# Kernel tuning notes

Hardware: AMD Instinct MI355X
Metric: run time of the kernel (lower is better)

## Reference

```python
import jax, jax.numpy as jnp
import numpy as np

B, N, D, H = 8, 2048, 768, 12
HD = D // H
SCALE = HD ** -0.5


def setup_inputs() -> dict:
    key = jax.random.key(0)
    ks = jax.random.split(key, 5)
    std = D ** -0.5
    return {
        "x": jax.random.normal(ks[0], (B, N, D), jnp.float32),
        "W_qkv": jax.random.normal(ks[1], (D, 3 * D), jnp.float32) * std,
        "b_qkv": jax.random.normal(ks[2], (3 * D,), jnp.float32) * 0.02,
        "W_out": jax.random.normal(ks[3], (D, D), jnp.float32) * std,
        "b_out": jax.random.normal(ks[4], (D,), jnp.float32) * 0.02,
    }


def reference(x, W_qkv, b_qkv, W_out, b_out):
    qkv = x @ W_qkv + b_qkv
    qkv = qkv.reshape(B, N, 3, H, HD).transpose(2, 0, 3, 1, 4)
    q, k, v = qkv[0], qkv[1], qkv[2]
    # scaled dot-product attention (dropout is identity in eval)
    attn = jnp.einsum("bhqd,bhkd->bhqk", q, k) * SCALE
    attn = jax.nn.softmax(attn, axis=-1)
    out = jnp.einsum("bhqk,bhkd->bhqd", attn, v)
    out = out.transpose(0, 2, 1, 3).reshape(B, N, D)
    return out @ W_out + b_out
```

## Files before the change

### kernel.cpp

```cpp
#include <hip/hip_runtime.h>
#include <hip/hip_bf16.h>
#include <stdint.h>

#define BB 8
#define NN 2048
#define DD 768
#define HH 12
#define HD 64
#define ND3 2304
#define TOK (BB*NN)
#define QSC 0.18033688011112042f

typedef __bf16 bf16x8 __attribute__((ext_vector_type(8)));
typedef float  f32x4  __attribute__((ext_vector_type(4)));
typedef float  f32x16 __attribute__((ext_vector_type(16)));
typedef unsigned uint2v __attribute__((ext_vector_type(2)));

__device__ __forceinline__ unsigned short f2bf(float f) {
    union { float f; unsigned u; } v; v.f = f;
    unsigned r = v.u + 0x7FFF + ((v.u >> 16) & 1);
    return (unsigned short)(r >> 16);
}
__device__ __forceinline__ unsigned packbf(float lo, float hi) {
    return __builtin_amdgcn_perm(__float_as_uint(hi) + 0x8000u,
                                 __float_as_uint(lo) + 0x8000u, 0x07060302u);
}
__device__ __forceinline__ unsigned cvtpk(float lo, float hi) {
    unsigned r;
    asm("v_cvt_pk_bf16_f32 %0, %1, %2" : "=v"(r) : "v"(lo), "v"(hi));
    return r;
}

__device__ __forceinline__ void gload_lds16(const unsigned short* g, unsigned short* l) {
    __builtin_amdgcn_global_load_lds((const __attribute__((address_space(1))) void*)g,
                                     (__attribute__((address_space(3))) void*)l, 16, 0, 0);
}

__global__ __launch_bounds__(256) void f32_to_bf16_vec(const float* __restrict__ in,
                                                       unsigned short* __restrict__ out, int n4) {
    int i = blockIdx.x * 256 + threadIdx.x;
    if (i < n4) {
        float4 v = reinterpret_cast<const float4*>(in)[i];
        ushort4 o;
        o.x = f2bf(v.x); o.y = f2bf(v.y); o.z = f2bf(v.z); o.w = f2bf(v.w);
        reinterpret_cast<ushort4*>(out)[i] = o;
    }
}

__global__ __launch_bounds__(256) void transpose_bf16_tiled(const float* __restrict__ in,
                                                            unsigned short* __restrict__ out,
                                                            int R, int C) {
    __shared__ float t[32][33];
    const int tid = threadIdx.x;
    const int tc = tid & 31;
    const int tr = tid >> 5;
    const int r0 = blockIdx.y * 32;
    const int c0 = blockIdx.x * 32;
    #pragma unroll
    for (int j = 0; j < 4; ++j)
        t[tr + j * 8][tc] = in[(size_t)(r0 + tr + j * 8) * C + c0 + tc];
    __syncthreads();
    #pragma unroll
    for (int j = 0; j < 4; ++j)
        out[(size_t)(c0 + tr + j * 8) * R + r0 + tc] = f2bf(t[tc][tr + j * 8]);
}

__global__ __launch_bounds__(256) void qkv_gemm(const unsigned short* __restrict__ xb,
                                                const unsigned short* __restrict__ wt,
                                                const float* __restrict__ bias,
                                                unsigned short* __restrict__ qb,
                                                unsigned short* __restrict__ kb,
                                                unsigned short* __restrict__ vt) {
    __shared__ __align__(16) unsigned short As[2][128 * 32];
    __shared__ __align__(16) unsigned short Bs[2][128 * 32];
    const int tid  = threadIdx.x;
    const int wave = tid >> 6;
    const int lane = tid & 63;
    const int qd   = lane >> 4;
    const int c    = lane & 15;

    const int nbx  = gridDim.x;
    const int nwg  = nbx * gridDim.y;
    const int orig = blockIdx.y * nbx + blockIdx.x;
    const int swz  = (orig & 7) * (nwg >> 3) + (orig >> 3);
    const int m0 = (swz / nbx) * 128;
    const int n0 = (swz % nbx) * 128;

    const int wm = (wave >> 1) * 64;
    const int wn = (wave & 1) * 64;

    const unsigned short* Ag = xb + (size_t)(m0 + wave * 32 + (lane >> 2)) * DD + (lane & 3) * 8;
    const unsigned short* Bg = wt + (size_t)(n0 + wave * 32 + (lane >> 2)) * DD + (lane & 3) * 8;
    const int rb = wave * 32;

    #pragma unroll
    for (int j = 0; j < 2; ++j) {
        gload_lds16(Ag + (size_t)(j * 16) * DD, &As[0][(rb + j * 16) * 32]);
        gload_lds16(Bg + (size_t)(j * 16) * DD, &Bs[0][(rb + j * 16) * 32]);
    }
    __syncthreads();

    f32x4 acc[4][4] = {};
    #pragma unroll 1
    for (int t = 0; t < DD / 32; ++t) {
        const int cur = t & 1;
        if (t + 1 < DD / 32) {
            const int k1 = (t + 1) * 32;
            #pragma unroll
            for (int j = 0; j < 2; ++j) {
                gload_lds16(Ag + (size_t)(j * 16) * DD + k1, &As[cur ^ 1][(rb + j * 16) * 32]);
                gload_lds16(Bg + (size_t)(j * 16) * DD + k1, &Bs[cur ^ 1][(rb + j * 16) * 32]);
            }
        }
        bf16x8 a[4], b[4];
        #pragma unroll
        for (int i = 0; i < 4; ++i)
            a[i] = *reinterpret_cast<const bf16x8*>(&As[cur][(wm + i * 16 + c) * 32 + qd * 8]);
        #pragma unroll
        for (int j = 0; j < 4; ++j)
            b[j] = *reinterpret_cast<const bf16x8*>(&Bs[cur][(wn + j * 16 + c) * 32 + qd * 8]);
        __builtin_amdgcn_s_setprio(1);
        #pragma unroll
        for (int i = 0; i < 4; ++i)
            #pragma unroll
            for (int j = 0; j < 4; ++j)
                acc[i][j] = __builtin_amdgcn_mfma_f32_16x16x32_bf16(a[i], b[j], acc[i][j], 0, 0, 0);
        __builtin_amdgcn_s_setprio(0);
        __syncthreads();
    }

    const int tt  = n0 / DD;
    const int cw  = n0 - tt * DD + wn;
    const int hh  = cw >> 6;
    const int rowb = m0 + wm;
    const int bi  = rowb >> 11;
    const int nb  = rowb & (NN - 1);
    const float scale = (tt == 0) ? QSC : 1.0f;

    unsigned short* W = (wave < 2) ? (&As[0][0] + wave * 4096)
                                   : (&Bs[0][0] + (wave - 2) * 4096);

    #pragma unroll
    for (int i = 0; i < 4; ++i)
        #pragma unroll
        for (int j = 0; j < 4; ++j)
            #pragma unroll
            for (int r = 0; r < 4; ++r) {
                int lr = i * 16 + qd * 4 + r;
                int lc = j * 16 + c;
                float v = (acc[i][j][r] + bias[n0 + wn + lc]) * scale;
                int rr  = (tt == 2) ? lc : lr;
                int ccl = (tt == 2) ? lr : lc;
                W[rr * 64 + ((((ccl >> 3) ^ (rr & 7)) << 3) | (ccl & 7))] = f2bf(v);
            }

    const int lr8 = lane >> 3;
    const int lch = lane & 7;
    unsigned short* dst0;
    size_t rstride;
    if (tt == 2) {
        dst0 = vt + ((size_t)(bi * HH + hh) * HD) * NN + nb + lch * 8;
        rstride = NN;
    } else {
        unsigned short* qk = (tt == 0) ? qb : kb;
        dst0 = qk + ((size_t)(bi * HH + hh) * NN + nb) * HD + lch * 8;
        rstride = HD;
    }
    #pragma unroll
    for (int s = 0; s < 8; ++s) {
        int rr  = s * 8 + lr8;
        int pch = lch ^ (rr & 7);
        uint4 val = *reinterpret_cast<const uint4*>(W + rr * 64 + pch * 8);
        *reinterpret_cast<uint4*>(dst0 + (size_t)rr * rstride) = val;
    }
}

__global__ __launch_bounds__(256, 4) void attn_kernel(const unsigned short* __restrict__ qb,
                                                      const unsigned short* __restrict__ kb,
                                                      const unsigned short* __restrict__ vt,
                                                      unsigned short* __restrict__ ao) {
    __shared__ __align__(16) unsigned short Ks[2][64 * HD];
    __shared__ __align__(16) unsigned short Vs[2][64 * HD];

    const int blk  = blockIdx.x;
    const int xcd  = blk & 7;
    const int g    = blk >> 3;
    const int bh   = xcd * 12 + (g >> 4);
    const int qt   = g & 15;
    const int tid  = threadIdx.x;
    const int wave = tid >> 6;
    const int lane = tid & 63;
    const int col  = lane & 31;
    const int hf   = lane >> 5;
    const int q0   = qt * 128 + wave * 32;

    const unsigned short* Qp = qb + (size_t)bh * NN * HD;
    const unsigned short* Kp = kb + (size_t)bh * NN * HD;
    const unsigned short* Vp = vt + (size_t)bh * HD * NN;

    const int srow = lane >> 3;
    const int sch  = (lane & 7) ^ srow;

    const int cswz = col & 7;
    const int o0 = col * 128 + ((0 + hf) ^ cswz) * 16;
    const int o1 = col * 128 + ((2 + hf) ^ cswz) * 16;
    const int o2 = col * 128 + ((4 + hf) ^ cswz) * 16;
    const int o3 = col * 128 + ((6 + hf) ^ cswz) * 16;

    bf16x8 aq[4];
    #pragma unroll
    for (int ks = 0; ks < 4; ++ks)
        aq[ks] = *reinterpret_cast<const bf16x8*>(Qp + (size_t)(q0 + col) * HD + ks * 16 + hf * 8);

    f32x16 ot[2] = {};
    f32x16 lacc  = {};
    const f32x16 zf = {};

    union { unsigned short u[8]; bf16x8 v; } onesb;
    #pragma unroll
    for (int i = 0; i < 8; ++i) onesb.u[i] = 0x3F80;

    #pragma unroll
    for (int j = 0; j < 2; ++j) {
        const int rb = wave * 16 + j * 8;
        gload_lds16(Kp + (size_t)(rb + srow) * HD + sch * 8, &Ks[0][rb * HD]);
        gload_lds16(Vp + (size_t)(rb + srow) * NN + sch * 8, &Vs[0][rb * HD]);
    }
    __syncthreads();

    #pragma unroll 1
    for (int kt = 0; kt < NN; kt += 64) {
        const int cur = (kt >> 6) & 1;

        if (kt + 64 < NN) {
            const int nb = cur ^ 1;
            #pragma unroll
            for (int j = 0; j < 2; ++j) {
                const int rb = wave * 16 + j * 8;
                gload_lds16(Kp + (size_t)(kt + 64 + rb + srow) * HD + sch * 8, &Ks[nb][rb * HD]);
                gload_lds16(Vp + (size_t)(rb + srow) * NN + kt + 64 + sch * 8, &Vs[nb][rb * HD]);
            }
        }

        const char* Ksb = (const char*)&Ks[cur][0];
        const char* Vsb = (const char*)&Vs[cur][0];

        bf16x8 kfa0 = *(const bf16x8*)(Ksb + o0);
        bf16x8 kfa1 = *(const bf16x8*)(Ksb + o1);
        bf16x8 kfa2 = *(const bf16x8*)(Ksb + o2);
        bf16x8 kfa3 = *(const bf16x8*)(Ksb + o3);
        __builtin_amdgcn_s_setprio(1);
        f32x16 s0;
        s0 = __builtin_amdgcn_mfma_f32_32x32x16_bf16(kfa0, aq[0], zf, 0, 0, 0);
        s0 = __builtin_amdgcn_mfma_f32_32x32x16_bf16(kfa1, aq[1], s0, 0, 0, 0);
        s0 = __builtin_amdgcn_mfma_f32_32x32x16_bf16(kfa2, aq[2], s0, 0, 0, 0);
        s0 = __builtin_amdgcn_mfma_f32_32x32x16_bf16(kfa3, aq[3], s0, 0, 0, 0);
        __builtin_amdgcn_s_setprio(0);

        bf16x8 kfb0 = *(const bf16x8*)(Ksb + o0 + 4096);
        bf16x8 kfb1 = *(const bf16x8*)(Ksb + o1 + 4096);
        bf16x8 kfb2 = *(const bf16x8*)(Ksb + o2 + 4096);
        bf16x8 kfb3 = *(const bf16x8*)(Ksb + o3 + 4096);

        unsigned pda[8];
        #pragma unroll
        for (int gi = 0; gi < 8; ++gi) {
            float p0 = __builtin_amdgcn_exp2f(s0[2 * gi]);
            float p1 = __builtin_amdgcn_exp2f(s0[2 * gi + 1]);
            pda[gi] = cvtpk(p0, p1);
        }

        __builtin_amdgcn_s_setprio(1);
        f32x16 s1;
        s1 = __builtin_amdgcn_mfma_f32_32x32x16_bf16(kfb0, aq[0], zf, 0, 0, 0);
        s1 = __builtin_amdgcn_mfma_f32_32x32x16_bf16(kfb1, aq[1], s1, 0, 0, 0);
        s1 = __builtin_amdgcn_mfma_f32_32x32x16_bf16(kfb2, aq[2], s1, 0, 0, 0);
        s1 = __builtin_amdgcn_mfma_f32_32x32x16_bf16(kfb3, aq[3], s1, 0, 0, 0);
        __builtin_amdgcn_s_setprio(0);

        unsigned pdb[8];
        #pragma unroll
        for (int gi = 0; gi < 8; ++gi) {
            float p0 = __builtin_amdgcn_exp2f(s1[2 * gi]);
            float p1 = __builtin_amdgcn_exp2f(s1[2 * gi + 1]);
            pdb[gi] = cvtpk(p0, p1);
        }

        #pragma unroll
        for (int kk = 0; kk < 4; ++kk) {
            const int bs = (kk & 1) * 4;
            const int oo = (kk == 0) ? o0 : (kk == 1) ? o1 : (kk == 2) ? o2 : o3;
            bf16x8 v0 = *(const bf16x8*)(Vsb + oo);
            bf16x8 v1 = *(const bf16x8*)(Vsb + oo + 4096);
            unsigned q0d = (kk < 2) ? pda[bs + 0] : pdb[bs + 0];
            unsigned q1d = (kk < 2) ? pda[bs + 1] : pdb[bs + 1];
            unsigned q2d = (kk < 2) ? pda[bs + 2] : pdb[bs + 2];
            unsigned q3d = (kk < 2) ? pda[bs + 3] : pdb[bs + 3];
            uint2v r02 = __builtin_amdgcn_permlane32_swap(q0d, q2d, false, false);
            uint2v r13 = __builtin_amdgcn_permlane32_swap(q1d, q3d, false, false);
            union { unsigned d[4]; bf16x8 v; } bfr;
            bfr.d[0] = r02.x;
            bfr.d[1] = r13.x;
            bfr.d[2] = r02.y;
            bfr.d[3] = r13.y;
            __builtin_amdgcn_s_setprio(1);
            ot[0] = __builtin_amdgcn_mfma_f32_32x32x16_bf16(v0, bfr.v, ot[0], 0, 0, 0);
            ot[1] = __builtin_amdgcn_mfma_f32_32x32x16_bf16(v1, bfr.v, ot[1], 0, 0, 0);
            lacc  = __builtin_amdgcn_mfma_f32_32x32x16_bf16(onesb.v, bfr.v, lacc, 0, 0, 0);
            __builtin_amdgcn_s_setprio(0);
        }

        __syncthreads();
    }

    float linv = 1.0f / lacc[0];
    const int bi = bh / HH;
    const int hh = bh - bi * HH;
    const int n  = q0 + col;
    size_t base = ((size_t)bi * NN + n) * DD + hh * HD;
    #pragma unroll
    for (int dt = 0; dt < 2; ++dt)
        #pragma unroll
        for (int g4 = 0; g4 < 4; ++g4) {
            uint2 dd2;
            dd2.x = packbf(ot[dt][4 * g4 + 0] * linv, ot[dt][4 * g4 + 1] * linv);
            dd2.y = packbf(ot[dt][4 * g4 + 2] * linv, ot[dt][4 * g4 + 3] * linv);
            *reinterpret_cast<uint2*>(&((unsigned short*)ao)[base + dt * 32 + g4 * 8 + hf * 4]) = dd2;
        }
}

__global__ __launch_bounds__(256) void out_gemm(const unsigned short* __restrict__ ab,
                                                const unsigned short* __restrict__ wt,
                                                const float* __restrict__ bias,
                                                float* __restrict__ out) {
    __shared__ __align__(16) unsigned short As[2][128 * 32];
    __shared__ __align__(16) unsigned short Bs[2][128 * 32];
    const int tid  = threadIdx.x;
    const int wave = tid >> 6;
    const int lane = tid & 63;
    const int qd   = lane >> 4;
    const int c    = lane & 15;

    const int nbx  = gridDim.x;
    const int nwg  = nbx * gridDim.y;
    const int orig = blockIdx.y * nbx + blockIdx.x;
    const int swz  = (orig & 7) * (nwg >> 3) + (orig >> 3);
    const int m0 = (swz / nbx) * 128;
    const int n0 = (swz % nbx) * 128;

    const int wm = (wave >> 1) * 64;
    const int wn = (wave & 1) * 64;

    const unsigned short* Ag = ab + (size_t)(m0 + wave * 32 + (lane >> 2)) * DD + (lane & 3) * 8;
    const unsigned short* Bg = wt + (size_t)(n0 + wave * 32 + (lane >> 2)) * DD + (lane & 3) * 8;
    const int rb = wave * 32;

    #pragma unroll
    for (int j = 0; j < 2; ++j) {
        gload_lds16(Ag + (size_t)(j * 16) * DD, &As[0][(rb + j * 16) * 32]);
        gload_lds16(Bg + (size_t)(j * 16) * DD, &Bs[0][(rb + j * 16) * 32]);
    }
    __syncthreads();

    f32x4 acc[4][4] = {};
    #pragma unroll 1
    for (int t = 0; t < DD / 32; ++t) {
        const int cur = t & 1;
        if (t + 1 < DD / 32) {
            const int k1 = (t + 1) * 32;
            #pragma unroll
            for (int j = 0; j < 2; ++j) {
                gload_lds16(Ag + (size_t)(j * 16) * DD + k1, &As[cur ^ 1][(rb + j * 16) * 32]);
                gload_lds16(Bg + (size_t)(j * 16) * DD + k1, &Bs[cur ^ 1][(rb + j * 16) * 32]);
            }
        }
        bf16x8 a[4], b[4];
        #pragma unroll
        for (int i = 0; i < 4; ++i)
            a[i] = *reinterpret_cast<const bf16x8*>(&As[cur][(wm + i * 16 + c) * 32 + qd * 8]);
        #pragma unroll
        for (int j = 0; j < 4; ++j)
            b[j] = *reinterpret_cast<const bf16x8*>(&Bs[cur][(wn + j * 16 + c) * 32 + qd * 8]);
        __builtin_amdgcn_s_setprio(1);
        #pragma unroll
        for (int i = 0; i < 4; ++i)
            #pragma unroll
            for (int j = 0; j < 4; ++j)
                acc[i][j] = __builtin_amdgcn_mfma_f32_16x16x32_bf16(a[i], b[j], acc[i][j], 0, 0, 0);
        __builtin_amdgcn_s_setprio(0);
        __syncthreads();
    }

    #pragma unroll
    for (int i = 0; i < 4; ++i)
        #pragma unroll
        for (int j = 0; j < 4; ++j)
            #pragma unroll
            for (int r = 0; r < 4; ++r) {
                int row = m0 + wm + i * 16 + qd * 4 + r;
                int col = n0 + wn + j * 16 + c;
                out[(size_t)row * DD + col] = acc[i][j][r] + bias[col];
            }
}

extern "C" void kernel_launch(void* const* d_in, const int* in_sizes, int n_in,
                              void* d_out, int out_size, void* d_ws, size_t ws_size,
                              hipStream_t stream) {
    const float* x     = (const float*)d_in[0];
    const float* W_qkv = (const float*)d_in[1];
    const float* b_qkv = (const float*)d_in[2];
    const float* W_out = (const float*)d_in[3];
    const float* b_out = (const float*)d_in[4];
    float* out = (float*)d_out;

    char* ws = (char*)d_ws;
    const size_t SZ_X   = (size_t)TOK * DD * 2;
    const size_t SZ_WQ  = (size_t)ND3 * DD * 2;
    const size_t SZ_WO  = (size_t)DD * DD * 2;
    const size_t SZ_QKV = (size_t)TOK * DD * 2;
    unsigned short* xb  = (unsigned short*)(ws);
    unsigned short* wtq = (unsigned short*)(ws + SZ_X);
    unsigned short* wto = (unsigned short*)(ws + SZ_X + SZ_WQ);
    unsigned short* qb  = (unsigned short*)(ws + SZ_X + SZ_WQ + SZ_WO);
    unsigned short* kb  = (unsigned short*)(ws + SZ_X + SZ_WQ + SZ_WO + SZ_QKV);
    unsigned short* vtb = (unsigned short*)(ws + SZ_X + SZ_WQ + SZ_WO + 2 * SZ_QKV);
    unsigned short* ao  = (unsigned short*)(ws + SZ_X + SZ_WQ + SZ_WO + 3 * SZ_QKV);

    {
        int n4 = TOK * DD / 4;
        f32_to_bf16_vec<<<(n4 + 255) / 256, 256, 0, stream>>>(x, xb, n4);
        transpose_bf16_tiled<<<dim3(ND3 / 32, DD / 32), 256, 0, stream>>>(W_qkv, wtq, DD, ND3);
        transpose_bf16_tiled<<<dim3(DD / 32, DD / 32), 256, 0, stream>>>(W_out, wto, DD, DD);
    }
    qkv_gemm<<<dim3(ND3 / 128, TOK / 128), 256, 0, stream>>>(xb, wtq, b_qkv, qb, kb, vtb);
    attn_kernel<<<1536, 256, 0, stream>>>(qb, kb, vtb, ao);
    out_gemm<<<dim3(DD / 128, TOK / 128), 256, 0, stream>>>(ao, wto, b_out, out);
}
```

Before: 347.3 us.

## Fuse prep kernels into one launch and triple-buffer QKV GEMM loads

Three preprocessing kernels (the x cast and the two weight transposes) become a single launch that dispatches on block index, removing two launch gaps. The QKV GEMM moves from double to triple buffering in LDS. It prefetches two k-tiles ahead, waits with explicit vmcnt counts, and issues one barrier per iteration instead of a trailing __syncthreads. LDS use rises from 32KB to 48KB per block, which may reduce occupancy. The hand-counted vmcnt waits assume exactly four outstanding loads per stage.

```diff
diff --git a/kernel.cpp b/kernel.cpp
--- a/kernel.cpp
+++ b/kernel.cpp
@@ -36,26 +36,38 @@
                                      (__attribute__((address_space(3))) void*)l, 16, 0, 0);
 }
 
-__global__ __launch_bounds__(256) void f32_to_bf16_vec(const float* __restrict__ in,
-                                                       unsigned short* __restrict__ out, int n4) {
-    int i = blockIdx.x * 256 + threadIdx.x;
-    if (i < n4) {
-        float4 v = reinterpret_cast<const float4*>(in)[i];
+#define NB_CAST 12288
+#define NB_TQ   1728
+#define NB_TO   576
+__global__ __launch_bounds__(256) void prep_all(const float* __restrict__ x,
+                                                unsigned short* __restrict__ xb,
+                                                const float* __restrict__ Wq,
+                                                unsigned short* __restrict__ wtq,
+                                                const float* __restrict__ Wo,
+                                                unsigned short* __restrict__ wto) {
+    __shared__ float t[32][33];
+    const int b   = blockIdx.x;
+    const int tid = threadIdx.x;
+    if (b < NB_CAST) {
+        int i = b * 256 + tid;
+        float4 v = reinterpret_cast<const float4*>(x)[i];
         ushort4 o;
         o.x = f2bf(v.x); o.y = f2bf(v.y); o.z = f2bf(v.z); o.w = f2bf(v.w);
-        reinterpret_cast<ushort4*>(out)[i] = o;
-    }
-}
-
-__global__ __launch_bounds__(256) void transpose_bf16_tiled(const float* __restrict__ in,
-                                                            unsigned short* __restrict__ out,
-                                                            int R, int C) {
-    __shared__ float t[32][33];
-    const int tid = threadIdx.x;
+        reinterpret_cast<ushort4*>(xb)[i] = o;
+        return;
+    }
+    const float* in;
+    unsigned short* out;
+    int R, C, id;
+    if (b < NB_CAST + NB_TQ) { in = Wq; out = wtq; R = DD; C = ND3; id = b - NB_CAST; }
+    else                     { in = Wo; out = wto; R = DD; C = DD;  id = b - NB_CAST - NB_TQ; }
+    const int ctiles = C >> 5;
+    const int cx = id % ctiles;
+    const int ry = id / ctiles;
+    const int r0 = ry * 32;
+    const int c0 = cx * 32;
     const int tc = tid & 31;
     const int tr = tid >> 5;
-    const int r0 = blockIdx.y * 32;
-    const int c0 = blockIdx.x * 32;
     #pragma unroll
     for (int j = 0; j < 4; ++j)
         t[tr + j * 8][tc] = in[(size_t)(r0 + tr + j * 8) * C + c0 + tc];
@@ -71,8 +83,8 @@
                                                 unsigned short* __restrict__ qb,
                                                 unsigned short* __restrict__ kb,
                                                 unsigned short* __restrict__ vt) {
-    __shared__ __align__(16) unsigned short As[2][128 * 32];
-    __shared__ __align__(16) unsigned short Bs[2][128 * 32];
+    __shared__ __align__(16) unsigned short As[3][128 * 32];
+    __shared__ __align__(16) unsigned short Bs[3][128 * 32];
     const int tid  = threadIdx.x;
     const int wave = tid >> 6;
     const int lane = tid & 63;
@@ -98,27 +110,35 @@
         gload_lds16(Ag + (size_t)(j * 16) * DD, &As[0][(rb + j * 16) * 32]);
         gload_lds16(Bg + (size_t)(j * 16) * DD, &Bs[0][(rb + j * 16) * 32]);
     }
-    __syncthreads();
-
+    #pragma unroll
+    for (int j = 0; j < 2; ++j) {
+        gload_lds16(Ag + (size_t)(j * 16) * DD + 32, &As[1][(rb + j * 16) * 32]);
+        gload_lds16(Bg + (size_t)(j * 16) * DD + 32, &Bs[1][(rb + j * 16) * 32]);
+    }
+
+    int c0i = 0, c1i = 1, c2i = 2;
     f32x4 acc[4][4] = {};
     #pragma unroll 1
     for (int t = 0; t < DD / 32; ++t) {
-        const int cur = t & 1;
-        if (t + 1 < DD / 32) {
-            const int k1 = (t + 1) * 32;
+        if (t < DD / 32 - 1) asm volatile("s_waitcnt vmcnt(4)" ::: "memory");
+        else                 asm volatile("s_waitcnt vmcnt(0)" ::: "memory");
+        __builtin_amdgcn_s_barrier();
+        __builtin_amdgcn_sched_barrier(0);
+        if (t + 2 < DD / 32) {
+            const int k2 = (t + 2) * 32;
             #pragma unroll
             for (int j = 0; j < 2; ++j) {
-                gload_lds16(Ag + (size_t)(j * 16) * DD + k1, &As[cur ^ 1][(rb + j * 16) * 32]);
-                gload_lds16(Bg + (size_t)(j * 16) * DD + k1, &Bs[cur ^ 1][(rb + j * 16) * 32]);
+                gload_lds16(Ag + (size_t)(j * 16) * DD + k2, &As[c2i][(rb + j * 16) * 32]);
+                gload_lds16(Bg + (size_t)(j * 16) * DD + k2, &Bs[c2i][(rb + j * 16) * 32]);
             }
         }
         bf16x8 a[4], b[4];
         #pragma unroll
         for (int i = 0; i < 4; ++i)
-            a[i] = *reinterpret_cast<const bf16x8*>(&As[cur][(wm + i * 16 + c) * 32 + qd * 8]);
+            a[i] = *reinterpret_cast<const bf16x8*>(&As[c0i][(wm + i * 16 + c) * 32 + qd * 8]);
         #pragma unroll
         for (int j = 0; j < 4; ++j)
-            b[j] = *reinterpret_cast<const bf16x8*>(&Bs[cur][(wn + j * 16 + c) * 32 + qd * 8]);
+            b[j] = *reinterpret_cast<const bf16x8*>(&Bs[c0i][(wn + j * 16 + c) * 32 + qd * 8]);
         __builtin_amdgcn_s_setprio(1);
         #pragma unroll
         for (int i = 0; i < 4; ++i)
@@ -126,8 +146,9 @@
             for (int j = 0; j < 4; ++j)
                 acc[i][j] = __builtin_amdgcn_mfma_f32_16x16x32_bf16(a[i], b[j], acc[i][j], 0, 0, 0);
         __builtin_amdgcn_s_setprio(0);
-        __syncthreads();
-    }
+        const int tmp = c0i; c0i = c1i; c1i = c2i; c2i = tmp;
+    }
+    __syncthreads();
 
     const int tt  = n0 / DD;
     const int cw  = n0 - tt * DD + wn;
@@ -426,12 +447,7 @@
     unsigned short* vtb = (unsigned short*)(ws + SZ_X + SZ_WQ + SZ_WO + 2 * SZ_QKV);
     unsigned short* ao  = (unsigned short*)(ws + SZ_X + SZ_WQ + SZ_WO + 3 * SZ_QKV);
 
-    {
-        int n4 = TOK * DD / 4;
-        f32_to_bf16_vec<<<(n4 + 255) / 256, 256, 0, stream>>>(x, xb, n4);
-        transpose_bf16_tiled<<<dim3(ND3 / 32, DD / 32), 256, 0, stream>>>(W_qkv, wtq, DD, ND3);
-        transpose_bf16_tiled<<<dim3(DD / 32, DD / 32), 256, 0, stream>>>(W_out, wto, DD, DD);
-    }
+    prep_all<<<NB_CAST + NB_TQ + NB_TO, 256, 0, stream>>>(x, xb, W_qkv, wtq, W_out, wto);
     qkv_gemm<<<dim3(ND3 / 128, TOK / 128), 256, 0, stream>>>(xb, wtq, b_qkv, qb, kb, vtb);
     attn_kernel<<<1536, 256, 0, stream>>>(qb, kb, vtb, ao);
     out_gemm<<<dim3(DD / 128, TOK / 128), 256, 0, stream>>>(ao, wto, b_out, out);
```

New measurement: 364.1 us. 1.05x slower.
